# Kernel optimization log

Measured on AMD Instinct MI355X. Metric: run time of the kernel, lower is better.

The kernel has to match this reference:

```python
import jax, jax.numpy as jnp
import numpy as np

N_NODES = 100000
N_FEAT = 512
HIDDEN = 256
N_CLASSES = 40
N_EDGES = 1600000
K = 10
ALPHA = 0.1


def setup_inputs() -> dict:
    key = jax.random.key(0)
    ks = jax.random.split(key, 8)
    feat = jax.random.normal(ks[0], (N_NODES, N_FEAT), dtype=jnp.float32)
    src = jax.random.randint(ks[1], (N_EDGES,), 0, N_NODES, dtype=jnp.int32)
    dst = jax.random.randint(ks[2], (N_EDGES,), 0, N_NODES, dtype=jnp.int32)
    # linear layers (PyTorch-style uniform init)
    s1 = 1.0 / np.sqrt(N_FEAT)
    W1 = jax.random.uniform(ks[3], (N_FEAT, HIDDEN), minval=-s1, maxval=s1, dtype=jnp.float32)
    b1 = jax.random.uniform(ks[4], (HIDDEN,), minval=-s1, maxval=s1, dtype=jnp.float32)
    s2 = 1.0 / np.sqrt(HIDDEN)
    W2 = jax.random.uniform(ks[5], (HIDDEN, N_CLASSES), minval=-s2, maxval=s2, dtype=jnp.float32)
    b2 = jax.random.uniform(ks[6], (N_CLASSES,), minval=-s2, maxval=s2, dtype=jnp.float32)
    # PPR init for per-hop weights: temp[k] = alpha*(1-alpha)^k, temp[K] = (1-alpha)^K
    temp = ALPHA * (1.0 - ALPHA) ** np.arange(K + 1)
    temp[-1] = (1.0 - ALPHA) ** K
    temp = jnp.asarray(temp, dtype=jnp.float32)
    return {"feat": feat, "W1": W1, "b1": b1, "W2": W2, "b2": b2,
            "temp": temp, "src": src, "dst": dst}


def reference(feat, W1, b1, W2, b2, temp, src, dst):
    N = feat.shape[0]
    # dgl.add_self_loop
    loop = jnp.arange(N, dtype=src.dtype)
    src_f = jnp.concatenate([src, loop])
    dst_f = jnp.concatenate([dst, loop])
    # MLP: lin1 -> relu -> lin2 (dropout is identity at inference)
    h = jax.nn.relu(feat @ W1 + b1) @ W2 + b2  # [N, C]
    # symmetric normalization: norm_e = d[dst] * d[src], d = deg^{-1/2}
    deg = jax.ops.segment_sum(jnp.ones_like(dst_f, dtype=h.dtype), dst_f, num_segments=N)
    d = jax.lax.rsqrt(deg)  # deg >= 1 due to self loops
    norm = (d[dst_f] * d[src_f])[:, None]  # [E, 1]
    # K-hop propagation with learned per-hop weights
    TH = h * temp[0]
    for k in range(K):
        msg = h[src_f] * norm                     # gather + edge scale
        h = jax.ops.segment_sum(msg, dst_f, num_segments=N)  # scatter-sum
        TH = TH + h * temp[k + 1]
    return jax.nn.log_softmax(TH, axis=1)
```

## Files before the change

kernel.cpp:

```cpp
#include <hip/hip_runtime.h>
#include <math.h>

#define N_NODES 100000
#define N_FEAT  512
#define HIDDEN  256
#define N_CLS   40
#define N_EDGES 1600000
#define K_HOPS  10
#define SCAN_BLOCKS 98
#define HPAD 64

typedef __attribute__((ext_vector_type(8))) short short8;
typedef __attribute__((ext_vector_type(4))) float f4_t;

__device__ __forceinline__ short f2bf(float f) {
    union { float f; unsigned u; } x; x.f = f;
    unsigned r = x.u + 0x7fffu + ((x.u >> 16) & 1u);
    return (short)(r >> 16);
}

__device__ __forceinline__ float bf2f(short b) {
    union { unsigned u; float f; } x;
    x.u = ((unsigned)(unsigned short)b) << 16;
    return x.f;
}


__global__ __launch_bounds__(256) void init_deg_kernel(int* __restrict__ deg) {
    int v = blockIdx.x * 256 + threadIdx.x;
    if (v < N_NODES) deg[v] = 1;
}

__global__ __launch_bounds__(256) void count_dst_kernel(const int* __restrict__ dst,
                                                        int* __restrict__ deg) {
    int e = blockIdx.x * 256 + threadIdx.x;
    if (e < N_EDGES) atomicAdd(&deg[dst[e]], 1);
}

__global__ __launch_bounds__(256) void rsqrt_deg_kernel(const int* __restrict__ deg,
                                                        float* __restrict__ d) {
    int v = blockIdx.x * 256 + threadIdx.x;
    if (v < N_NODES) d[v] = rsqrtf((float)deg[v]);
}


__global__ __launch_bounds__(1024) void scan_partial_kernel(const int* __restrict__ deg,
                                                            int* __restrict__ blocksum) {
    __shared__ int s[1024];
    int t = threadIdx.x;
    int idx = blockIdx.x * 1024 + t;
    s[t] = (idx < N_NODES) ? deg[idx] : 0;
    __syncthreads();
#pragma unroll
    for (int off = 512; off > 0; off >>= 1) {
        if (t < off) s[t] += s[t + off];
        __syncthreads();
    }
    if (t == 0) blocksum[blockIdx.x] = s[0];
}

__global__ __launch_bounds__(64) void scan_blocks_kernel(const int* __restrict__ blocksum,
                                                         int* __restrict__ blockoff) {
    if (threadIdx.x == 0) {
        int run = 0;
        for (int b = 0; b < SCAN_BLOCKS; ++b) { blockoff[b] = run; run += blocksum[b]; }
    }
}

__global__ __launch_bounds__(1024) void scan_write_kernel(const int* __restrict__ deg,
                                                          const int* __restrict__ blockoff,
                                                          int* __restrict__ rowptr,
                                                          int* __restrict__ cursor) {
    __shared__ int s[1024];
    int t = threadIdx.x;
    int idx = blockIdx.x * 1024 + t;
    int v = (idx < N_NODES) ? deg[idx] : 0;
    s[t] = v;
    __syncthreads();
#pragma unroll
    for (int off = 1; off < 1024; off <<= 1) {
        int add = (t >= off) ? s[t - off] : 0;
        __syncthreads();
        s[t] += add;
        __syncthreads();
    }
    int pre = s[t] - v + blockoff[blockIdx.x];
    if (idx <= N_NODES) rowptr[idx] = pre;
    if (idx < N_NODES) cursor[idx] = pre;
}

__global__ __launch_bounds__(256) void scatter_edges_kernel(const int* __restrict__ src,
                                                            const int* __restrict__ dst,
                                                            const float* __restrict__ d,
                                                            int* __restrict__ cursor,
                                                            int2* __restrict__ epair) {
    int e = blockIdx.x * 256 + threadIdx.x;
    if (e >= N_EDGES) return;
    int u = src[e], v = dst[e];
    int pos = atomicAdd(&cursor[v], 1);
    int2 p;
    p.x = u;
    p.y = __float_as_int(d[u] * d[v]);
    epair[pos] = p;
}

__global__ __launch_bounds__(256) void scatter_self_kernel(const float* __restrict__ d,
                                                           int* __restrict__ cursor,
                                                           int2* __restrict__ epair) {
    int v = blockIdx.x * 256 + threadIdx.x;
    if (v >= N_NODES) return;
    int pos = atomicAdd(&cursor[v], 1);
    float dv = d[v];
    int2 p;
    p.x = v;
    p.y = __float_as_int(dv * dv);
    epair[pos] = p;
}

__global__ __launch_bounds__(256) void cvt_w1_kernel(const float* __restrict__ W1,
                                                     short* __restrict__ W1T) {
    int lin = blockIdx.x * 256 + threadIdx.x;
    int k = lin >> 8, n = lin & 255;
    W1T[n * 512 + k] = f2bf(W1[lin]);
}

__global__ __launch_bounds__(256) void cvt_w2_kernel(const float* __restrict__ W2,
                                                     short* __restrict__ W2T) {
    int lin = blockIdx.x * 256 + threadIdx.x;
    int n = lin >> 8, k = lin & 255;
    W2T[lin] = (n < N_CLS) ? f2bf(W2[k * N_CLS + n]) : (short)0;
}

__global__ __launch_bounds__(256) void mlp_kernel(const float* __restrict__ feat,
                                                  const short* __restrict__ W1T,
                                                  const float* __restrict__ b1,
                                                  const short* __restrict__ W2T,
                                                  const float* __restrict__ b2,
                                                  const float* __restrict__ temp,
                                                  short* __restrict__ h,
                                                  float* __restrict__ TH) {
    __shared__ union {
        struct { short A[64][72]; short B[256][72]; } a;
        short W2s[48][264];
    } uS;
    __shared__ short sH[64][264];

    const int tid = threadIdx.x;
    const int rbase = blockIdx.x * 64;
    const int lane = tid & 63;
    const int wv = tid >> 6;
    const int quad = lane >> 4;
    const int l15 = lane & 15;

    f4_t acc[4][4];
#pragma unroll
    for (int m = 0; m < 4; ++m)
#pragma unroll
        for (int n = 0; n < 4; ++n) acc[m][n] = (f4_t)0.f;

    const int arow = tid >> 2;
    const int akq = tid & 3;
    for (int kt = 0; kt < 8; ++kt) {
        __syncthreads();
        {
            int grow = rbase + arow;
            f4_t f0 = (f4_t)0.f, f1 = (f4_t)0.f, f2 = (f4_t)0.f, f3 = (f4_t)0.f;
            if (grow < N_NODES) {
                const f4_t* p = (const f4_t*)(feat + grow * N_FEAT + kt * 64 + akq * 16);
                f0 = p[0]; f1 = p[1]; f2 = p[2]; f3 = p[3];
            }
            short8 lo, hi;
            lo[0]=f2bf(f0[0]); lo[1]=f2bf(f0[1]); lo[2]=f2bf(f0[2]); lo[3]=f2bf(f0[3]);
            lo[4]=f2bf(f1[0]); lo[5]=f2bf(f1[1]); lo[6]=f2bf(f1[2]); lo[7]=f2bf(f1[3]);
            hi[0]=f2bf(f2[0]); hi[1]=f2bf(f2[1]); hi[2]=f2bf(f2[2]); hi[3]=f2bf(f2[3]);
            hi[4]=f2bf(f3[0]); hi[5]=f2bf(f3[1]); hi[6]=f2bf(f3[2]); hi[7]=f2bf(f3[3]);
            short8* dstp = (short8*)&uS.a.A[arow][akq * 16];
            dstp[0] = lo; dstp[1] = hi;
        }
#pragma unroll
        for (int p = 0; p < 8; ++p) {
            int lin = p * 256 + tid;
            int col = lin >> 3, kc = lin & 7;
            *(short8*)&uS.a.B[col][kc * 8] =
                *(const short8*)(W1T + col * 512 + kt * 64 + kc * 8);
        }
        __syncthreads();
#pragma unroll
        for (int kk = 0; kk < 64; kk += 32) {
            short8 af[4], bf[4];
#pragma unroll
            for (int m = 0; m < 4; ++m)
                af[m] = *(const short8*)&uS.a.A[m * 16 + l15][kk + quad * 8];
#pragma unroll
            for (int n = 0; n < 4; ++n)
                bf[n] = *(const short8*)&uS.a.B[wv * 64 + n * 16 + l15][kk + quad * 8];
#pragma unroll
            for (int m = 0; m < 4; ++m)
#pragma unroll
                for (int n = 0; n < 4; ++n)
                    acc[m][n] = __builtin_amdgcn_mfma_f32_16x16x32_bf16(af[m], bf[n],
                                                                        acc[m][n], 0, 0, 0);
        }
    }
    __syncthreads();

#pragma unroll
    for (int n = 0; n < 4; ++n) {
        int col = wv * 64 + n * 16 + l15;
        float bb = b1[col];
#pragma unroll
        for (int m = 0; m < 4; ++m)
#pragma unroll
            for (int r = 0; r < 4; ++r) {
                float v = acc[m][n][r] + bb;
                sH[m * 16 + quad * 4 + r][col] = f2bf(v > 0.f ? v : 0.f);
            }
    }
#pragma unroll
    for (int p = 0; p < 6; ++p) {
        int lin = p * 256 + tid;
        int n = lin >> 5, kc = lin & 31;
        *(short8*)&uS.W2s[n][kc * 8] = *(const short8*)(W2T + n * 256 + kc * 8);
    }
    __syncthreads();

    f4_t accB[3];
#pragma unroll
    for (int n = 0; n < 3; ++n) accB[n] = (f4_t)0.f;
#pragma unroll
    for (int kk = 0; kk < 256; kk += 32) {
        short8 a = *(const short8*)&sH[wv * 16 + l15][kk + quad * 8];
#pragma unroll
        for (int n = 0; n < 3; ++n) {
            short8 b = *(const short8*)&uS.W2s[n * 16 + l15][kk + quad * 8];
            accB[n] = __builtin_amdgcn_mfma_f32_16x16x32_bf16(a, b, accB[n], 0, 0, 0);
        }
    }
    float t0 = temp[0];
#pragma unroll
    for (int n = 0; n < 3; ++n) {
        int col = n * 16 + l15;
        if (col < N_CLS) {
            float bb = b2[col];
#pragma unroll
            for (int r = 0; r < 4; ++r) {
                int grow = rbase + wv * 16 + quad * 4 + r;
                if (grow < N_NODES) {
                    float v = accB[n][r] + bb;
                    h[grow * HPAD + col] = f2bf(v);
                    TH[grow * N_CLS + col] = t0 * v;
                }
            }
        }
    }
}

__global__ __launch_bounds__(256) void prop_kernel(const short* __restrict__ h,
                                                   short* __restrict__ hn,
                                                   const int* __restrict__ rowptr,
                                                   const int2* __restrict__ epair,
                                                   float* __restrict__ TH,
                                                   const float* __restrict__ temp,
                                                   int kidx) {
    int gid = blockIdx.x * 256 + threadIdx.x;
    int v = gid / 5;
    if (v >= N_NODES) return;
    int c = gid - v * 5;
    int s = rowptr[v], e = rowptr[v + 1];
    f4_t a0 = (f4_t)0.f, a1 = (f4_t)0.f;
    int j = s;
    for (; j + 4 <= e; j += 4) {
        int2 e0 = epair[j], e1 = epair[j + 1], e2 = epair[j + 2], e3 = epair[j + 3];
        short8 h0 = *(const short8*)(h + e0.x * HPAD + c * 8);
        short8 h1 = *(const short8*)(h + e1.x * HPAD + c * 8);
        short8 h2 = *(const short8*)(h + e2.x * HPAD + c * 8);
        short8 h3 = *(const short8*)(h + e3.x * HPAD + c * 8);
        float w0 = __int_as_float(e0.y), w1 = __int_as_float(e1.y);
        float w2 = __int_as_float(e2.y), w3 = __int_as_float(e3.y);
#pragma unroll
        for (int i = 0; i < 4; ++i) {
            a0[i] += w0 * bf2f(h0[i]) + w1 * bf2f(h1[i]) + w2 * bf2f(h2[i]) + w3 * bf2f(h3[i]);
            a1[i] += w0 * bf2f(h0[4 + i]) + w1 * bf2f(h1[4 + i]) + w2 * bf2f(h2[4 + i]) +
                     w3 * bf2f(h3[4 + i]);
        }
    }
    for (; j < e; ++j) {
        int2 ep = epair[j];
        short8 hb = *(const short8*)(h + ep.x * HPAD + c * 8);
        float w = __int_as_float(ep.y);
#pragma unroll
        for (int i = 0; i < 4; ++i) {
            a0[i] += w * bf2f(hb[i]);
            a1[i] += w * bf2f(hb[4 + i]);
        }
    }
    float tk = temp[kidx];
    short8 ob;
#pragma unroll
    for (int i = 0; i < 4; ++i) { ob[i] = f2bf(a0[i]); ob[4 + i] = f2bf(a1[i]); }
    *(short8*)(hn + v * HPAD + c * 8) = ob;
    f4_t* pt = (f4_t*)(TH + v * N_CLS + c * 8);
    pt[0] += tk * a0;
    pt[1] += tk * a1;
}

__global__ __launch_bounds__(256) void lsm_kernel(float* __restrict__ out) {
    int wid = (blockIdx.x * 256 + threadIdx.x) >> 6;
    int lane = threadIdx.x & 63;
    if (wid >= N_NODES) return;
    float x = (lane < N_CLS) ? out[wid * N_CLS + lane] : -INFINITY;
    float m = x;
#pragma unroll
    for (int o = 32; o > 0; o >>= 1) m = fmaxf(m, __shfl_xor(m, o, 64));
    float e = (lane < N_CLS) ? expf(x - m) : 0.f;
    float s = e;
#pragma unroll
    for (int o = 32; o > 0; o >>= 1) s += __shfl_xor(s, o, 64);
    float r = x - m - logf(s);
    if (lane < N_CLS) out[wid * N_CLS + lane] = r;
}


extern "C" void kernel_launch(void* const* d_in, const int* in_sizes, int n_in,
                              void* d_out, int out_size, void* d_ws, size_t ws_size,
                              hipStream_t stream) {
    const float* feat = (const float*)d_in[0];
    const float* W1   = (const float*)d_in[1];
    const float* b1   = (const float*)d_in[2];
    const float* W2   = (const float*)d_in[3];
    const float* b2   = (const float*)d_in[4];
    const float* temp = (const float*)d_in[5];
    const int*   src  = (const int*)d_in[6];
    const int*   dst  = (const int*)d_in[7];
    float* out = (float*)d_out;

    char* ws = (char*)d_ws;
    int*   deg    = (int*)(ws + 0);
    short* W1T    = (short*)(ws + 0);
    short* W2T    = (short*)(ws + 262144);
    float* dnorm  = (float*)(ws + 400000);
    int*   rowptr = (int*)(ws + 800000);
    int*   cursor = (int*)(ws + 1200016);
    int2*  epair  = (int2*)(ws + 1600032);
    short* h0     = (short*)(ws + 15200032);
    short* h1     = (short*)(ws + 28000032);
    int*   blocksum = (int*)(ws + 40800032);
    int*   blockoff = (int*)(ws + 40800432);

    init_deg_kernel<<<(N_NODES + 255) / 256, 256, 0, stream>>>(deg);
    count_dst_kernel<<<(N_EDGES + 255) / 256, 256, 0, stream>>>(dst, deg);
    rsqrt_deg_kernel<<<(N_NODES + 255) / 256, 256, 0, stream>>>(deg, dnorm);
    scan_partial_kernel<<<SCAN_BLOCKS, 1024, 0, stream>>>(deg, blocksum);
    scan_blocks_kernel<<<1, 64, 0, stream>>>(blocksum, blockoff);
    scan_write_kernel<<<SCAN_BLOCKS, 1024, 0, stream>>>(deg, blockoff, rowptr, cursor);
    cvt_w1_kernel<<<512, 256, 0, stream>>>(W1, W1T);
    cvt_w2_kernel<<<64, 256, 0, stream>>>(W2, W2T);
    scatter_edges_kernel<<<(N_EDGES + 255) / 256, 256, 0, stream>>>(src, dst, dnorm, cursor,
                                                                    epair);
    scatter_self_kernel<<<(N_NODES + 255) / 256, 256, 0, stream>>>(dnorm, cursor, epair);

    mlp_kernel<<<(N_NODES + 63) / 64, 256, 0, stream>>>(feat, W1T, b1, W2T, b2, temp, h0, out);

    short* hc = h0;
    short* hn = h1;
    for (int k = 0; k < K_HOPS; ++k) {
        prop_kernel<<<(N_NODES * 5 + 255) / 256, 256, 0, stream>>>(hc, hn, rowptr, epair,
                                                                   out, temp, k + 1);
        short* t = hc; hc = hn; hn = t;
    }

    lsm_kernel<<<(N_NODES / 4), 256, 0, stream>>>(out);
}
```

Before: 893.3 us.

## Split propagation features into per-XCD planes so gathers stay L2-resident

Stores the bf16 hidden state as 8 separate planes of 5 classes each (16-byte rows) instead of one 64-wide padded row per node. The propagation kernel now gives each thread one node and one plane, and interleaves planes by blockIdx & 7. With round-robin block dispatch, each XCD's random gathers should then hit a small per-plane working set in its L2 instead of the full hidden array. In exchange every plane re-reads the edge list and row pointers, 3 of every 8 stored values are padding, and the TH update becomes narrower strided scalar accesses.

```diff
diff --git a/kernel.cpp b/kernel.cpp
--- a/kernel.cpp
+++ b/kernel.cpp
@@ -8,7 +8,7 @@
 #define N_EDGES 1600000
 #define K_HOPS  10
 #define SCAN_BLOCKS 98
-#define HPAD 64
+#define PLANE   (N_NODES * 8)
 
 typedef __attribute__((ext_vector_type(8))) short short8;
 typedef __attribute__((ext_vector_type(4))) float f4_t;
@@ -242,12 +242,14 @@
         int col = n * 16 + l15;
         if (col < N_CLS) {
             float bb = b2[col];
+            int plane = col / 5;
+            int ci = col - plane * 5;
 #pragma unroll
             for (int r = 0; r < 4; ++r) {
                 int grow = rbase + wv * 16 + quad * 4 + r;
                 if (grow < N_NODES) {
                     float v = accB[n][r] + bb;
-                    h[grow * HPAD + col] = f2bf(v);
+                    h[plane * PLANE + grow * 8 + ci] = f2bf(v);
                     TH[grow * N_CLS + col] = t0 * v;
                 }
             }
@@ -262,46 +264,48 @@
                                                    float* __restrict__ TH,
                                                    const float* __restrict__ temp,
                                                    int kidx) {
-    int gid = blockIdx.x * 256 + threadIdx.x;
-    int v = gid / 5;
+    const int g = blockIdx.x & 7;
+    const int v = (blockIdx.x >> 3) * 256 + threadIdx.x;
     if (v >= N_NODES) return;
-    int c = gid - v * 5;
+    const short* hp = h + g * PLANE;
     int s = rowptr[v], e = rowptr[v + 1];
-    f4_t a0 = (f4_t)0.f, a1 = (f4_t)0.f;
+    float a0 = 0.f, a1 = 0.f, a2 = 0.f, a3 = 0.f, a4 = 0.f;
     int j = s;
     for (; j + 4 <= e; j += 4) {
-        int2 e0 = epair[j], e1 = epair[j + 1], e2 = epair[j + 2], e3 = epair[j + 3];
-        short8 h0 = *(const short8*)(h + e0.x * HPAD + c * 8);
-        short8 h1 = *(const short8*)(h + e1.x * HPAD + c * 8);
-        short8 h2 = *(const short8*)(h + e2.x * HPAD + c * 8);
-        short8 h3 = *(const short8*)(h + e3.x * HPAD + c * 8);
-        float w0 = __int_as_float(e0.y), w1 = __int_as_float(e1.y);
-        float w2 = __int_as_float(e2.y), w3 = __int_as_float(e3.y);
-#pragma unroll
-        for (int i = 0; i < 4; ++i) {
-            a0[i] += w0 * bf2f(h0[i]) + w1 * bf2f(h1[i]) + w2 * bf2f(h2[i]) + w3 * bf2f(h3[i]);
-            a1[i] += w0 * bf2f(h0[4 + i]) + w1 * bf2f(h1[4 + i]) + w2 * bf2f(h2[4 + i]) +
-                     w3 * bf2f(h3[4 + i]);
-        }
+        int2 p0 = epair[j], p1 = epair[j + 1], p2 = epair[j + 2], p3 = epair[j + 3];
+        short8 x0 = *(const short8*)(hp + p0.x * 8);
+        short8 x1 = *(const short8*)(hp + p1.x * 8);
+        short8 x2 = *(const short8*)(hp + p2.x * 8);
+        short8 x3 = *(const short8*)(hp + p3.x * 8);
+        float w0 = __int_as_float(p0.y), w1 = __int_as_float(p1.y);
+        float w2 = __int_as_float(p2.y), w3 = __int_as_float(p3.y);
+        a0 += w0 * bf2f(x0[0]) + w1 * bf2f(x1[0]) + w2 * bf2f(x2[0]) + w3 * bf2f(x3[0]);
+        a1 += w0 * bf2f(x0[1]) + w1 * bf2f(x1[1]) + w2 * bf2f(x2[1]) + w3 * bf2f(x3[1]);
+        a2 += w0 * bf2f(x0[2]) + w1 * bf2f(x1[2]) + w2 * bf2f(x2[2]) + w3 * bf2f(x3[2]);
+        a3 += w0 * bf2f(x0[3]) + w1 * bf2f(x1[3]) + w2 * bf2f(x2[3]) + w3 * bf2f(x3[3]);
+        a4 += w0 * bf2f(x0[4]) + w1 * bf2f(x1[4]) + w2 * bf2f(x2[4]) + w3 * bf2f(x3[4]);
     }
     for (; j < e; ++j) {
-        int2 ep = epair[j];
-        short8 hb = *(const short8*)(h + ep.x * HPAD + c * 8);
-        float w = __int_as_float(ep.y);
-#pragma unroll
-        for (int i = 0; i < 4; ++i) {
-            a0[i] += w * bf2f(hb[i]);
-            a1[i] += w * bf2f(hb[4 + i]);
-        }
+        int2 p = epair[j];
+        short8 x = *(const short8*)(hp + p.x * 8);
+        float w = __int_as_float(p.y);
+        a0 += w * bf2f(x[0]);
+        a1 += w * bf2f(x[1]);
+        a2 += w * bf2f(x[2]);
+        a3 += w * bf2f(x[3]);
+        a4 += w * bf2f(x[4]);
     }
     float tk = temp[kidx];
     short8 ob;
-#pragma unroll
-    for (int i = 0; i < 4; ++i) { ob[i] = f2bf(a0[i]); ob[4 + i] = f2bf(a1[i]); }
-    *(short8*)(hn + v * HPAD + c * 8) = ob;
-    f4_t* pt = (f4_t*)(TH + v * N_CLS + c * 8);
+    ob[0] = f2bf(a0); ob[1] = f2bf(a1); ob[2] = f2bf(a2); ob[3] = f2bf(a3); ob[4] = f2bf(a4);
+    ob[5] = 0; ob[6] = 0; ob[7] = 0;
+    *(short8*)(hn + g * PLANE + v * 8) = ob;
+    float* pt = TH + v * N_CLS + g * 5;
     pt[0] += tk * a0;
     pt[1] += tk * a1;
+    pt[2] += tk * a2;
+    pt[3] += tk * a3;
+    pt[4] += tk * a4;
 }
 
 __global__ __launch_bounds__(256) void lsm_kernel(float* __restrict__ out) {
@@ -361,11 +365,11 @@
 
     mlp_kernel<<<(N_NODES + 63) / 64, 256, 0, stream>>>(feat, W1T, b1, W2T, b2, temp, h0, out);
 
+    const int NB = (N_NODES + 255) / 256;
     short* hc = h0;
     short* hn = h1;
     for (int k = 0; k < K_HOPS; ++k) {
-        prop_kernel<<<(N_NODES * 5 + 255) / 256, 256, 0, stream>>>(hc, hn, rowptr, epair,
-                                                                   out, temp, k + 1);
+        prop_kernel<<<NB * 8, 256, 0, stream>>>(hc, hn, rowptr, epair, out, temp, k + 1);
         short* t = hc; hc = hn; hn = t;
     }
 
```

After: 1.727 ms. +93.4%, slower.
